# Optimization experiments

Measured on AMD Instinct MI355X. Metric: run time of the kernel, lower is better.

The kernel has to match this reference:

```python
import jax, jax.numpy as jnp
import numpy as np

B, T, DIM, HID = 8, 2048, 1024, 128

def setup_inputs() -> dict:
    key = jax.random.key(0)
    ks = jax.random.split(key, 6)
    x = jax.random.normal(ks[0], (B, T, DIM), dtype=jnp.float32)
    wk_w = jax.random.normal(ks[1], (DIM, HID), dtype=jnp.float32) * 0.02
    wk_b = jnp.zeros((HID,), dtype=jnp.float32)
    wv_w = jax.random.normal(ks[2], (DIM, HID), dtype=jnp.float32) * 0.02
    wv_b = jnp.zeros((HID,), dtype=jnp.float32)
    # xavier_uniform for w [T,T]: bound = sqrt(6/(T+T))
    bound = float(np.sqrt(6.0 / (T + T)))
    w = jax.random.uniform(ks[3], (T, T), dtype=jnp.float32, minval=-bound, maxval=bound)
    return {"x": x, "wk_w": wk_w, "wk_b": wk_b, "wv_w": wv_w, "wv_b": wv_b, "w": w}

def reference(x, wk_w, wk_b, wv_w, wv_b, w):
    # K, V projections: [B,T,HID]
    K = x @ wk_w + wk_b
    V = x @ wv_w + wv_b
    eK = jnp.exp(K)            # [B,T,HID]
    ew = jnp.exp(w)            # [T,T], shared left operand of both matmuls
    num = jnp.einsum('ts,bsh->bth', ew, eK * V)  # exp(w) @ (exp(K)*V)
    den = jnp.einsum('ts,bsh->bth', ew, eK)      # exp(w) @ exp(K)
    # Original module returns `weighted` (before sigmoid(Q) gating and ffnn)
    return num / den
```

## Files before the change

kernel.cpp:

```cpp
#include <hip/hip_runtime.h>
#include <hip/hip_bf16.h>


#define T_    2048
#define DIM_  1024
#define HID_  128

typedef __attribute__((ext_vector_type(8))) __bf16 bf16x8;
typedef __attribute__((ext_vector_type(4))) float f32x4;
typedef __attribute__((ext_vector_type(4))) unsigned short us4;
typedef __attribute__((ext_vector_type(8))) unsigned short us8;

typedef const unsigned int __attribute__((address_space(1)))* gas_t;
typedef unsigned int __attribute__((address_space(3)))* las_t;

__device__ __forceinline__ unsigned short f2bf(float f) {
    unsigned int u = __builtin_bit_cast(unsigned int, f);
    u += 0x7fffu + ((u >> 16) & 1u);
    return (unsigned short)(u >> 16);
}

__device__ __forceinline__ void gload16(const void* g, void* l) {
    __builtin_amdgcn_global_load_lds((gas_t)g, (las_t)l, 16, 0, 0);
}

__global__ __launch_bounds__(256) void prep_ew(const float* __restrict__ w,
                                               unsigned short* __restrict__ ew) {
    int idx = blockIdx.x * 256 + threadIdx.x;
    f32x4 v = ((const f32x4*)w)[idx];
    us4 o;
    o[0] = f2bf(__expf(v[0]));
    o[1] = f2bf(__expf(v[1]));
    o[2] = f2bf(__expf(v[2]));
    o[3] = f2bf(__expf(v[3]));
    ((us4*)ew)[idx] = o;
}

__global__ __launch_bounds__(256) void prep_wkv(const float* __restrict__ wk,
                                                const float* __restrict__ wv,
                                                unsigned short* __restrict__ wkvT) {
    int t = blockIdx.x * 256 + threadIdx.x;
    int n = t & 255, k = t >> 8;
    float v = (n < 128) ? wk[k * 128 + n] : wv[k * 128 + (n - 128)];
    wkvT[n * 1024 + k] = f2bf(v);
}

__global__ __launch_bounds__(256) void gemm1(const float* __restrict__ x,
                                             const unsigned short* __restrict__ wkvT,
                                             const float* __restrict__ wk_b,
                                             const float* __restrict__ wv_b,
                                             unsigned short* __restrict__ KVc) {
    __shared__ __align__(16) unsigned short As[2][64 * 72];
    __shared__ __align__(16) unsigned short Bs[2][256 * 64];
    const int tid  = threadIdx.x;
    const int m0   = blockIdx.x * 64;
    const int bb   = m0 >> 11;
    const int t0   = m0 & (T_ - 1);
    const int wave = tid >> 6, lane = tid & 63;
    const int lr = lane & 15, lq = lane >> 4;

    f32x4 acc[4][4];
#pragma unroll
    for (int i = 0; i < 4; i++)
#pragma unroll
        for (int j = 0; j < 4; j++) acc[i][j] = {0.f, 0.f, 0.f, 0.f};

    f32x4 areg[4];
#pragma unroll
    for (int i = 0; i < 4; i++) {
        int c = i * 256 + tid, r = c >> 4, c4 = (c & 15) * 4;
        areg[i] = *(const f32x4*)(x + (size_t)(m0 + r) * DIM_ + c4);
    }
#pragma unroll
    for (int i = 0; i < 8; i++) {
        int c = i * 256 + tid, r = c >> 3, kc = ((c & 7) ^ (r & 7)) * 8;
        gload16(wkvT + (size_t)r * DIM_ + kc, &Bs[0][(i * 256 + wave * 64) * 8]);
    }
#pragma unroll
    for (int i = 0; i < 4; i++) {
        int c = i * 256 + tid, r = c >> 4, c4 = (c & 15) * 4;
        us4 o;
        o[0] = f2bf(areg[i][0]); o[1] = f2bf(areg[i][1]);
        o[2] = f2bf(areg[i][2]); o[3] = f2bf(areg[i][3]);
        *(us4*)(&As[0][r * 72 + c4]) = o;
    }
    __syncthreads();

    int buf = 0;
    for (int t = 0; t < 16; t++) {
        if (t < 15) {
            int k0 = (t + 1) * 64;
#pragma unroll
            for (int i = 0; i < 4; i++) {
                int c = i * 256 + tid, r = c >> 4, c4 = (c & 15) * 4;
                areg[i] = *(const f32x4*)(x + (size_t)(m0 + r) * DIM_ + k0 + c4);
            }
#pragma unroll
            for (int i = 0; i < 8; i++) {
                int c = i * 256 + tid, r = c >> 3, kc = ((c & 7) ^ (r & 7)) * 8;
                gload16(wkvT + (size_t)r * DIM_ + k0 + kc,
                        &Bs[buf ^ 1][(i * 256 + wave * 64) * 8]);
            }
        }
#pragma unroll
        for (int ks = 0; ks < 64; ks += 32) {
            bf16x8 af[4], bfr[4];
#pragma unroll
            for (int mf = 0; mf < 4; mf++)
                af[mf] = *(const bf16x8*)(&As[buf][(mf * 16 + lr) * 72 + ks + lq * 8]);
#pragma unroll
            for (int nf = 0; nf < 4; nf++) {
                int rb = (nf < 2) ? (wave * 32 + nf * 16 + lr)
                                  : (128 + wave * 32 + (nf - 2) * 16 + lr);
                bfr[nf] = *(const bf16x8*)(&Bs[buf][rb * 64 + ((ks + lq * 8) ^ ((rb & 7) << 3))]);
            }
#pragma unroll
            for (int mf = 0; mf < 4; mf++)
#pragma unroll
                for (int nf = 0; nf < 4; nf++)
                    acc[mf][nf] = __builtin_amdgcn_mfma_f32_16x16x32_bf16(
                        af[mf], bfr[nf], acc[mf][nf], 0, 0, 0);
        }
        if (t < 15) {
#pragma unroll
            for (int i = 0; i < 4; i++) {
                int c = i * 256 + tid, r = c >> 4, c4 = (c & 15) * 4;
                us4 o;
                o[0] = f2bf(areg[i][0]); o[1] = f2bf(areg[i][1]);
                o[2] = f2bf(areg[i][2]); o[3] = f2bf(areg[i][3]);
                *(us4*)(&As[buf ^ 1][r * 72 + c4]) = o;
            }
        }
        __syncthreads();
        buf ^= 1;
    }

    unsigned short* ekvS = &Bs[0][0];
    unsigned short* ekS  = ekvS + 128 * 72;
#pragma unroll
    for (int nf = 0; nf < 2; nf++) {
        int h = wave * 32 + nf * 16 + lr;
        float bk = wk_b[h], bv = wv_b[h];
#pragma unroll
        for (int mf = 0; mf < 4; mf++) {
            int m = mf * 16 + lq * 4;
            us4 ok, okv;
#pragma unroll
            for (int j = 0; j < 4; j++) {
                float ek = __expf(acc[mf][nf][j] + bk);
                float vv = acc[mf][nf + 2][j] + bv;
                ok[j]  = f2bf(ek);
                okv[j] = f2bf(ek * vv);
            }
            *(us4*)(ekS  + h * 72 + m) = ok;
            *(us4*)(ekvS + h * 72 + m) = okv;
        }
    }
    __syncthreads();
    unsigned short* dst = KVc + (size_t)bb * 256 * T_;
#pragma unroll
    for (int i = 0; i < 4; i++) {
        int c = i * 256 + tid;
        int h = c >> 3, mc = (c & 7) * 8;
        us8 vkv = *(const us8*)(ekvS + h * 72 + mc);
        us8 vk  = *(const us8*)(ekS  + h * 72 + mc);
        *(us8*)(dst + (size_t)h * T_ + t0 + mc)         = vkv;
        *(us8*)(dst + (size_t)(128 + h) * T_ + t0 + mc) = vk;
    }
}

__global__ __launch_bounds__(256) void gemm2(const unsigned short* __restrict__ ew,
                                             const unsigned short* __restrict__ KVc,
                                             float* __restrict__ out) {
    __shared__ __align__(16) unsigned short As[2][64 * 64];
    __shared__ __align__(16) unsigned short Bs[2][256 * 64];
    const int tid  = threadIdx.x;
    const int t0   = blockIdx.x * 64;
    const int b    = blockIdx.y;
    const unsigned short* Bsrc = KVc + (size_t)b * 256 * T_;
    const int wave = tid >> 6, lane = tid & 63;
    const int lr = lane & 15, lq = lane >> 4;

    f32x4 acc[4][4];
#pragma unroll
    for (int i = 0; i < 4; i++)
#pragma unroll
        for (int j = 0; j < 4; j++) acc[i][j] = {0.f, 0.f, 0.f, 0.f};

#pragma unroll
    for (int i = 0; i < 2; i++) {
        int c = i * 256 + tid, r = c >> 3, kc = ((c & 7) ^ (r & 7)) * 8;
        gload16(ew + (size_t)(t0 + r) * T_ + kc, &As[0][(i * 256 + wave * 64) * 8]);
    }
#pragma unroll
    for (int i = 0; i < 8; i++) {
        int c = i * 256 + tid, r = c >> 3, kc = ((c & 7) ^ (r & 7)) * 8;
        gload16(Bsrc + (size_t)r * T_ + kc, &Bs[0][(i * 256 + wave * 64) * 8]);
    }
    __syncthreads();

    int buf = 0;
    for (int t = 0; t < 32; t++) {
        if (t < 31) {
            int k0 = (t + 1) * 64;
#pragma unroll
            for (int i = 0; i < 2; i++) {
                int c = i * 256 + tid, r = c >> 3, kc = ((c & 7) ^ (r & 7)) * 8;
                gload16(ew + (size_t)(t0 + r) * T_ + k0 + kc,
                        &As[buf ^ 1][(i * 256 + wave * 64) * 8]);
            }
#pragma unroll
            for (int i = 0; i < 8; i++) {
                int c = i * 256 + tid, r = c >> 3, kc = ((c & 7) ^ (r & 7)) * 8;
                gload16(Bsrc + (size_t)r * T_ + k0 + kc,
                        &Bs[buf ^ 1][(i * 256 + wave * 64) * 8]);
            }
        }
#pragma unroll
        for (int ks = 0; ks < 64; ks += 32) {
            bf16x8 af[4], bfr[4];
#pragma unroll
            for (int mf = 0; mf < 4; mf++) {
                int ra = mf * 16 + lr;
                af[mf] = *(const bf16x8*)(&As[buf][ra * 64 + ((ks + lq * 8) ^ ((ra & 7) << 3))]);
            }
#pragma unroll
            for (int nf = 0; nf < 4; nf++) {
                int rb = (nf < 2) ? (wave * 32 + nf * 16 + lr)
                                  : (128 + wave * 32 + (nf - 2) * 16 + lr);
                bfr[nf] = *(const bf16x8*)(&Bs[buf][rb * 64 + ((ks + lq * 8) ^ ((rb & 7) << 3))]);
            }
#pragma unroll
            for (int mf = 0; mf < 4; mf++)
#pragma unroll
                for (int nf = 0; nf < 4; nf++)
                    acc[mf][nf] = __builtin_amdgcn_mfma_f32_16x16x32_bf16(
                        af[mf], bfr[nf], acc[mf][nf], 0, 0, 0);
        }
        __syncthreads();
        buf ^= 1;
    }

    float* ob = out + ((size_t)b * T_ + t0) * HID_;
#pragma unroll
    for (int nf = 0; nf < 2; nf++) {
        int h = wave * 32 + nf * 16 + lr;
#pragma unroll
        for (int mf = 0; mf < 4; mf++) {
            int m = mf * 16 + lq * 4;
#pragma unroll
            for (int j = 0; j < 4; j++)
                ob[(size_t)(m + j) * HID_ + h] = acc[mf][nf][j] / acc[mf][nf + 2][j];
        }
    }
}

extern "C" void kernel_launch(void* const* d_in, const int* in_sizes, int n_in,
                              void* d_out, int out_size, void* d_ws, size_t ws_size,
                              hipStream_t stream) {
    const float* x    = (const float*)d_in[0];
    const float* wk_w = (const float*)d_in[1];
    const float* wk_b = (const float*)d_in[2];
    const float* wv_w = (const float*)d_in[3];
    const float* wv_b = (const float*)d_in[4];
    const float* w    = (const float*)d_in[5];

    char* ws = (char*)d_ws;
    unsigned short* ws_ew   = (unsigned short*)(ws);
    unsigned short* ws_wkvT = (unsigned short*)(ws + (8u << 20));
    unsigned short* ws_KVc  = (unsigned short*)(ws + (9u << 20));

    prep_ew  <<<4096, 256, 0, stream>>>(w, ws_ew);
    prep_wkv <<<1024, 256, 0, stream>>>(wk_w, wv_w, ws_wkvT);
    gemm1    <<<256, 256, 0, stream>>>(x, ws_wkvT, wk_b, wv_b, ws_KVc);
    gemm2    <<<dim3(32, 8), 256, 0, stream>>>(ws_ew, ws_KVc, (float*)d_out);
}
```

Measured before the change: 183.7 us.

## Halve M tile to 32 and drop LDS double buffering in both GEMMs

Both GEMM kernels now process 32 rows per block instead of 64, doubling the grid (512 blocks for gemm1, 64x8 for gemm2). The aim is to fill the 256 CUs of MI355X better, since the old grids gave one block per CU or less. LDS double buffering and register prefetch are removed in favour of a single buffer with sync-load-sync per K step. That cuts LDS use and raises occupancy, but it serialises loads and MFMA within a block and doubles reloads of the shared B tile (wkvT / KVc) across blocks.

```diff
diff --git a/kernel.cpp b/kernel.cpp
--- a/kernel.cpp
+++ b/kernel.cpp
@@ -50,99 +50,74 @@
                                              const float* __restrict__ wk_b,
                                              const float* __restrict__ wv_b,
                                              unsigned short* __restrict__ KVc) {
-    __shared__ __align__(16) unsigned short As[2][64 * 72];
-    __shared__ __align__(16) unsigned short Bs[2][256 * 64];
+    __shared__ __align__(16) unsigned short As[32 * 72];
+    __shared__ __align__(16) unsigned short Bs[256 * 64];
     const int tid  = threadIdx.x;
-    const int m0   = blockIdx.x * 64;
+    const int m0   = blockIdx.x * 32;
     const int bb   = m0 >> 11;
     const int t0   = m0 & (T_ - 1);
     const int wave = tid >> 6, lane = tid & 63;
     const int lr = lane & 15, lq = lane >> 4;
 
-    f32x4 acc[4][4];
-#pragma unroll
-    for (int i = 0; i < 4; i++)
+    f32x4 acc[2][4];
+#pragma unroll
+    for (int i = 0; i < 2; i++)
 #pragma unroll
         for (int j = 0; j < 4; j++) acc[i][j] = {0.f, 0.f, 0.f, 0.f};
 
-    f32x4 areg[4];
-#pragma unroll
-    for (int i = 0; i < 4; i++) {
-        int c = i * 256 + tid, r = c >> 4, c4 = (c & 15) * 4;
-        areg[i] = *(const f32x4*)(x + (size_t)(m0 + r) * DIM_ + c4);
-    }
-#pragma unroll
-    for (int i = 0; i < 8; i++) {
-        int c = i * 256 + tid, r = c >> 3, kc = ((c & 7) ^ (r & 7)) * 8;
-        gload16(wkvT + (size_t)r * DIM_ + kc, &Bs[0][(i * 256 + wave * 64) * 8]);
-    }
-#pragma unroll
-    for (int i = 0; i < 4; i++) {
-        int c = i * 256 + tid, r = c >> 4, c4 = (c & 15) * 4;
-        us4 o;
-        o[0] = f2bf(areg[i][0]); o[1] = f2bf(areg[i][1]);
-        o[2] = f2bf(areg[i][2]); o[3] = f2bf(areg[i][3]);
-        *(us4*)(&As[0][r * 72 + c4]) = o;
-    }
-    __syncthreads();
-
-    int buf = 0;
     for (int t = 0; t < 16; t++) {
-        if (t < 15) {
-            int k0 = (t + 1) * 64;
-#pragma unroll
-            for (int i = 0; i < 4; i++) {
-                int c = i * 256 + tid, r = c >> 4, c4 = (c & 15) * 4;
-                areg[i] = *(const f32x4*)(x + (size_t)(m0 + r) * DIM_ + k0 + c4);
-            }
-#pragma unroll
-            for (int i = 0; i < 8; i++) {
-                int c = i * 256 + tid, r = c >> 3, kc = ((c & 7) ^ (r & 7)) * 8;
-                gload16(wkvT + (size_t)r * DIM_ + k0 + kc,
-                        &Bs[buf ^ 1][(i * 256 + wave * 64) * 8]);
-            }
-        }
+        int k0 = t * 64;
+        __syncthreads();
+#pragma unroll
+        for (int i = 0; i < 8; i++) {
+            int c = i * 256 + tid, r = c >> 3, kc = ((c & 7) ^ (r & 7)) * 8;
+            gload16(wkvT + (size_t)r * DIM_ + k0 + kc, &Bs[(i * 256 + wave * 64) * 8]);
+        }
+        f32x4 areg[2];
+#pragma unroll
+        for (int i = 0; i < 2; i++) {
+            int c = i * 256 + tid, r = c >> 4, c4 = (c & 15) * 4;
+            areg[i] = *(const f32x4*)(x + (size_t)(m0 + r) * DIM_ + k0 + c4);
+        }
+#pragma unroll
+        for (int i = 0; i < 2; i++) {
+            int c = i * 256 + tid, r = c >> 4, c4 = (c & 15) * 4;
+            us4 o;
+            o[0] = f2bf(areg[i][0]); o[1] = f2bf(areg[i][1]);
+            o[2] = f2bf(areg[i][2]); o[3] = f2bf(areg[i][3]);
+            *(us4*)(&As[r * 72 + c4]) = o;
+        }
+        __syncthreads();
 #pragma unroll
         for (int ks = 0; ks < 64; ks += 32) {
-            bf16x8 af[4], bfr[4];
-#pragma unroll
-            for (int mf = 0; mf < 4; mf++)
-                af[mf] = *(const bf16x8*)(&As[buf][(mf * 16 + lr) * 72 + ks + lq * 8]);
+            bf16x8 af[2], bfr[4];
+#pragma unroll
+            for (int mf = 0; mf < 2; mf++)
+                af[mf] = *(const bf16x8*)(&As[(mf * 16 + lr) * 72 + ks + lq * 8]);
 #pragma unroll
             for (int nf = 0; nf < 4; nf++) {
                 int rb = (nf < 2) ? (wave * 32 + nf * 16 + lr)
                                   : (128 + wave * 32 + (nf - 2) * 16 + lr);
-                bfr[nf] = *(const bf16x8*)(&Bs[buf][rb * 64 + ((ks + lq * 8) ^ ((rb & 7) << 3))]);
-            }
-#pragma unroll
-            for (int mf = 0; mf < 4; mf++)
+                bfr[nf] = *(const bf16x8*)(&Bs[rb * 64 + ((ks + lq * 8) ^ ((rb & 7) << 3))]);
+            }
+#pragma unroll
+            for (int mf = 0; mf < 2; mf++)
 #pragma unroll
                 for (int nf = 0; nf < 4; nf++)
                     acc[mf][nf] = __builtin_amdgcn_mfma_f32_16x16x32_bf16(
                         af[mf], bfr[nf], acc[mf][nf], 0, 0, 0);
         }
-        if (t < 15) {
-#pragma unroll
-            for (int i = 0; i < 4; i++) {
-                int c = i * 256 + tid, r = c >> 4, c4 = (c & 15) * 4;
-                us4 o;
-                o[0] = f2bf(areg[i][0]); o[1] = f2bf(areg[i][1]);
-                o[2] = f2bf(areg[i][2]); o[3] = f2bf(areg[i][3]);
-                *(us4*)(&As[buf ^ 1][r * 72 + c4]) = o;
-            }
-        }
-        __syncthreads();
-        buf ^= 1;
-    }
-
-    unsigned short* ekvS = &Bs[0][0];
-    unsigned short* ekS  = ekvS + 128 * 72;
+    }
+
+    __syncthreads();
+    unsigned short* ekvS = &Bs[0];
+    unsigned short* ekS  = ekvS + 128 * 40;
 #pragma unroll
     for (int nf = 0; nf < 2; nf++) {
         int h = wave * 32 + nf * 16 + lr;
         float bk = wk_b[h], bv = wv_b[h];
 #pragma unroll
-        for (int mf = 0; mf < 4; mf++) {
+        for (int mf = 0; mf < 2; mf++) {
             int m = mf * 16 + lq * 4;
             us4 ok, okv;
 #pragma unroll
@@ -152,18 +127,18 @@
                 ok[j]  = f2bf(ek);
                 okv[j] = f2bf(ek * vv);
             }
-            *(us4*)(ekS  + h * 72 + m) = ok;
-            *(us4*)(ekvS + h * 72 + m) = okv;
+            *(us4*)(ekS  + h * 40 + m) = ok;
+            *(us4*)(ekvS + h * 40 + m) = okv;
         }
     }
     __syncthreads();
     unsigned short* dst = KVc + (size_t)bb * 256 * T_;
 #pragma unroll
-    for (int i = 0; i < 4; i++) {
+    for (int i = 0; i < 2; i++) {
         int c = i * 256 + tid;
-        int h = c >> 3, mc = (c & 7) * 8;
-        us8 vkv = *(const us8*)(ekvS + h * 72 + mc);
-        us8 vk  = *(const us8*)(ekS  + h * 72 + mc);
+        int h = c >> 2, mc = (c & 3) * 8;
+        us8 vkv = *(const us8*)(ekvS + h * 40 + mc);
+        us8 vk  = *(const us8*)(ekS  + h * 40 + mc);
         *(us8*)(dst + (size_t)h * T_ + t0 + mc)         = vkv;
         *(us8*)(dst + (size_t)(128 + h) * T_ + t0 + mc) = vk;
     }
@@ -172,73 +147,55 @@
 __global__ __launch_bounds__(256) void gemm2(const unsigned short* __restrict__ ew,
                                              const unsigned short* __restrict__ KVc,
                                              float* __restrict__ out) {
-    __shared__ __align__(16) unsigned short As[2][64 * 64];
-    __shared__ __align__(16) unsigned short Bs[2][256 * 64];
+    __shared__ __align__(16) unsigned short As[32 * 64];
+    __shared__ __align__(16) unsigned short Bs[256 * 64];
     const int tid  = threadIdx.x;
-    const int t0   = blockIdx.x * 64;
+    const int t0   = blockIdx.x * 32;
     const int b    = blockIdx.y;
     const unsigned short* Bsrc = KVc + (size_t)b * 256 * T_;
     const int wave = tid >> 6, lane = tid & 63;
     const int lr = lane & 15, lq = lane >> 4;
 
-    f32x4 acc[4][4];
-#pragma unroll
-    for (int i = 0; i < 4; i++)
+    f32x4 acc[2][4];
+#pragma unroll
+    for (int i = 0; i < 2; i++)
 #pragma unroll
         for (int j = 0; j < 4; j++) acc[i][j] = {0.f, 0.f, 0.f, 0.f};
 
-#pragma unroll
-    for (int i = 0; i < 2; i++) {
-        int c = i * 256 + tid, r = c >> 3, kc = ((c & 7) ^ (r & 7)) * 8;
-        gload16(ew + (size_t)(t0 + r) * T_ + kc, &As[0][(i * 256 + wave * 64) * 8]);
-    }
-#pragma unroll
-    for (int i = 0; i < 8; i++) {
-        int c = i * 256 + tid, r = c >> 3, kc = ((c & 7) ^ (r & 7)) * 8;
-        gload16(Bsrc + (size_t)r * T_ + kc, &Bs[0][(i * 256 + wave * 64) * 8]);
-    }
-    __syncthreads();
-
-    int buf = 0;
     for (int t = 0; t < 32; t++) {
-        if (t < 31) {
-            int k0 = (t + 1) * 64;
-#pragma unroll
-            for (int i = 0; i < 2; i++) {
-                int c = i * 256 + tid, r = c >> 3, kc = ((c & 7) ^ (r & 7)) * 8;
-                gload16(ew + (size_t)(t0 + r) * T_ + k0 + kc,
-                        &As[buf ^ 1][(i * 256 + wave * 64) * 8]);
-            }
-#pragma unroll
-            for (int i = 0; i < 8; i++) {
-                int c = i * 256 + tid, r = c >> 3, kc = ((c & 7) ^ (r & 7)) * 8;
-                gload16(Bsrc + (size_t)r * T_ + k0 + kc,
-                        &Bs[buf ^ 1][(i * 256 + wave * 64) * 8]);
-            }
-        }
+        int k0 = t * 64;
+        __syncthreads();
+        {
+            int c = tid, r = c >> 3, kc = ((c & 7) ^ (r & 7)) * 8;
+            gload16(ew + (size_t)(t0 + r) * T_ + k0 + kc, &As[(wave * 64) * 8]);
+        }
+#pragma unroll
+        for (int i = 0; i < 8; i++) {
+            int c = i * 256 + tid, r = c >> 3, kc = ((c & 7) ^ (r & 7)) * 8;
+            gload16(Bsrc + (size_t)r * T_ + k0 + kc, &Bs[(i * 256 + wave * 64) * 8]);
+        }
+        __syncthreads();
 #pragma unroll
         for (int ks = 0; ks < 64; ks += 32) {
-            bf16x8 af[4], bfr[4];
-#pragma unroll
-            for (int mf = 0; mf < 4; mf++) {
+            bf16x8 af[2], bfr[4];
+#pragma unroll
+            for (int mf = 0; mf < 2; mf++) {
                 int ra = mf * 16 + lr;
-                af[mf] = *(const bf16x8*)(&As[buf][ra * 64 + ((ks + lq * 8) ^ ((ra & 7) << 3))]);
+                af[mf] = *(const bf16x8*)(&As[ra * 64 + ((ks + lq * 8) ^ ((ra & 7) << 3))]);
             }
 #pragma unroll
             for (int nf = 0; nf < 4; nf++) {
                 int rb = (nf < 2) ? (wave * 32 + nf * 16 + lr)
                                   : (128 + wave * 32 + (nf - 2) * 16 + lr);
-                bfr[nf] = *(const bf16x8*)(&Bs[buf][rb * 64 + ((ks + lq * 8) ^ ((rb & 7) << 3))]);
-            }
-#pragma unroll
-            for (int mf = 0; mf < 4; mf++)
+                bfr[nf] = *(const bf16x8*)(&Bs[rb * 64 + ((ks + lq * 8) ^ ((rb & 7) << 3))]);
+            }
+#pragma unroll
+            for (int mf = 0; mf < 2; mf++)
 #pragma unroll
                 for (int nf = 0; nf < 4; nf++)
                     acc[mf][nf] = __builtin_amdgcn_mfma_f32_16x16x32_bf16(
                         af[mf], bfr[nf], acc[mf][nf], 0, 0, 0);
         }
-        __syncthreads();
-        buf ^= 1;
     }
 
     float* ob = out + ((size_t)b * T_ + t0) * HID_;
@@ -246,7 +203,7 @@
     for (int nf = 0; nf < 2; nf++) {
         int h = wave * 32 + nf * 16 + lr;
 #pragma unroll
-        for (int mf = 0; mf < 4; mf++) {
+        for (int mf = 0; mf < 2; mf++) {
             int m = mf * 16 + lq * 4;
 #pragma unroll
             for (int j = 0; j < 4; j++)
@@ -272,6 +229,6 @@
 
     prep_ew  <<<4096, 256, 0, stream>>>(w, ws_ew);
     prep_wkv <<<1024, 256, 0, stream>>>(wk_w, wv_w, ws_wkvT);
-    gemm1    <<<256, 256, 0, stream>>>(x, ws_wkvT, wk_b, wv_b, ws_KVc);
-    gemm2    <<<dim3(32, 8), 256, 0, stream>>>(ws_ew, ws_KVc, (float*)d_out);
-}
+    gemm1    <<<512, 256, 0, stream>>>(x, ws_wkvT, wk_b, wv_b, ws_KVc);
+    gemm2    <<<dim3(64, 8), 256, 0, stream>>>(ws_ew, ws_KVc, (float*)d_out);
+}
```

Result: faster. 168.0 us (-8.5%).
